# Kernel optimization log

Measured on AMD Instinct MI355X. Metric: run time of the kernel, lower is better.

Reference implementation:

```python
import jax, jax.numpy as jnp
import numpy as np

N_HEADS, D_MODEL, D_HEAD = 12, 768, 64
INIT_RANGE = 0.02
IGNORE = -100000.0

def setup_inputs() -> dict:
    key = jax.random.key(0)
    ks = jax.random.split(key, 5)
    x = jax.random.normal(ks[0], (4, 2048, D_MODEL), dtype=jnp.float32)
    W_Q = jax.random.normal(ks[1], (N_HEADS, D_MODEL, D_HEAD), dtype=jnp.float32) * INIT_RANGE
    W_K = jax.random.normal(ks[2], (N_HEADS, D_MODEL, D_HEAD), dtype=jnp.float32) * INIT_RANGE
    W_V = jax.random.normal(ks[3], (N_HEADS, D_MODEL, D_HEAD), dtype=jnp.float32) * INIT_RANGE
    W_O = jax.random.normal(ks[4], (N_HEADS, D_HEAD, D_MODEL), dtype=jnp.float32) * INIT_RANGE
    b_Q = jnp.zeros((N_HEADS, D_HEAD), dtype=jnp.float32)
    b_K = jnp.zeros((N_HEADS, D_HEAD), dtype=jnp.float32)
    b_V = jnp.zeros((N_HEADS, D_HEAD), dtype=jnp.float32)
    b_O = jnp.zeros((D_MODEL,), dtype=jnp.float32)
    return {"normalized_resid_pre": x, "W_Q": W_Q, "b_Q": b_Q, "W_K": W_K,
            "b_K": b_K, "W_V": W_V, "b_V": b_V, "W_O": W_O, "b_O": b_O}

def reference(normalized_resid_pre, W_Q, b_Q, W_K, b_K, W_V, b_V, W_O, b_O):
    x = normalized_resid_pre  # [b, s, d_model]
    q = jnp.einsum('bsd,hde->bshe', x, W_Q) + b_Q  # [b, s, h, d_head]
    k = jnp.einsum('bsd,hde->bshe', x, W_K) + b_K
    v = jnp.einsum('bsd,hde->bshe', x, W_V) + b_V
    scores = jnp.einsum('bqhe,bkhe->bhqk', q, k) / jnp.sqrt(jnp.float32(D_HEAD))
    S = x.shape[1]
    causal = jnp.triu(jnp.ones((S, S), dtype=bool), k=1)  # True above diagonal
    scores = jnp.where(causal, jnp.float32(IGNORE), scores)
    pattern = jax.nn.softmax(scores, axis=-1)  # [b, h, q, k]
    z = jnp.einsum('bhqk,bkhe->bqhe', pattern, v)
    attn_out = jnp.einsum('bqhe,hed->bqd', z, W_O) + b_O
    return attn_out
```

## Files before the change

kernel.cpp:

```cpp
#include <hip/hip_runtime.h>

typedef unsigned short u16;
typedef __bf16 bf16x8 __attribute__((ext_vector_type(8)));
typedef float f32x4 __attribute__((ext_vector_type(4)));

#define D_MODEL 768
#define NH 12
#define SEQ 2048
#define BB 4
#define QSCALE 0.18033688011112042f
#define FIXM 8.0f

__device__ __forceinline__ u16 f2b(float f) {
  __bf16 h = (__bf16)f;
  return __builtin_bit_cast(u16, h);
}

__device__ __forceinline__ void gload16(const void* g, void* l) {
  __builtin_amdgcn_global_load_lds((__attribute__((address_space(1))) void*)g,
                                   (__attribute__((address_space(3))) void*)l, 16, 0, 0);
}

__device__ __forceinline__ f32x4 mm16(bf16x8 a, bf16x8 b, f32x4 c) {
  return __builtin_amdgcn_mfma_f32_16x16x32_bf16(a, b, c, 0, 0, 0);
}

__global__ void prep_kernel(const float* __restrict__ x, const float* __restrict__ wq,
                            const float* __restrict__ wk, const float* __restrict__ wv,
                            const float* __restrict__ wo, const float* __restrict__ bq,
                            const float* __restrict__ bk, const float* __restrict__ bv,
                            u16* __restrict__ xb, u16* __restrict__ wt,
                            u16* __restrict__ wot, float* __restrict__ qkvb) {
  const int bid = blockIdx.x;
  if (bid < 6144) {
    int i = (bid * 256 + threadIdx.x) * 4;
    float4 v = *(const float4*)&x[i];
    ushort4 o;
    o.x = f2b(v.x); o.y = f2b(v.y); o.z = f2b(v.z); o.w = f2b(v.w);
    *(ushort4*)&xb[i] = o;
  } else {
    int i = (bid - 6144) * 256 + threadIdx.x;
    {
      int cp = i / 768, d = i % 768;
      int proj = cp / 768, c = cp % 768, h = c / 64, e = c % 64;
      const float* W = (proj == 0) ? wq : ((proj == 1) ? wk : wv);
      float v = W[(size_t)h * 49152 + d * 64 + e];
      if (proj == 0) v *= QSCALE;
      wt[i] = f2b(v);
    }
    if (i < 768 * 768) {
      int rp = i / 768, d = i % 768;
      wot[i] = f2b(wo[(size_t)d * 768 + rp]);
    }
    if (i < 2304) {
      int proj = i / 768, c = i % 768;
      float v = (proj == 0) ? bq[c] * QSCALE : ((proj == 1) ? bk[c] : bv[c]);
      qkvb[i] = v;
    }
  }
}

__global__ __launch_bounds__(512) void gemm_qkv_kernel(
    const u16* __restrict__ A, const u16* __restrict__ Bt,
    const float* __restrict__ qkvb, u16* __restrict__ qw, u16* __restrict__ kw,
    u16* __restrict__ vw) {
  __shared__ u16 lds[73728];
  const int tid = threadIdx.x;
  const int w = tid >> 6, lane = tid & 63;
  const int lg = lane >> 4, cl = lane & 15;
  const int L = blockIdx.x;
  const int v = (L & 7) * 72 + (L >> 3);
  const int bm = v % 9, bn = v / 9;
  const int wr = w >> 1, wc = w & 1;
  const int NT = 12;

  f32x4 vzero = {0.f, 0.f, 0.f, 0.f};
  f32x4 acc[4][4];
#pragma unroll
  for (int mi = 0; mi < 4; mi++)
#pragma unroll
    for (int ni = 0; ni < 4; ni++) acc[mi][ni] = vzero;

  const u16* aB = A + (size_t)bm * 256 * D_MODEL;
  const u16* bB = Bt + (size_t)bn * 128 * D_MODEL;
  const int l8 = lane >> 3, l7 = lane & 7;
  const int c7 = cl & 7;
  const int sw7 = l7 ^ l8;

  auto stage = [&](int buf, int kt, int half) {
    const int kof = kt * 64;
#pragma unroll
    for (int j2 = 0; j2 < 2; j2++) {
      const int r0 = (w * 4 + half * 2 + j2) * 8;
      gload16(aB + (size_t)(r0 + l8) * D_MODEL + kof + sw7 * 8,
              &lds[buf * 16384 + r0 * 64]);
    }
    const int r0b = (w * 2 + half) * 8;
    gload16(bB + (size_t)(r0b + l8) * D_MODEL + kof + sw7 * 8,
            &lds[49152 + buf * 8192 + r0b * 64]);
  };

  stage(0, 0, 0); stage(0, 0, 1);
  stage(1, 1, 0); stage(1, 1, 1);
  asm volatile("s_waitcnt vmcnt(6)" ::: "memory");
  __builtin_amdgcn_s_barrier();

  for (int kt = 0; kt < NT; ++kt) {
    const int cA = (kt % 3) * 16384;
    const int cB = 49152 + (kt % 3) * 8192;
    const int nbuf = (kt + 2) % 3;
#pragma unroll
    for (int ks = 0; ks < 2; ks++) {
      const int kc = (ks * 4 + lg) ^ c7;
      bf16x8 af[4], bf4[4];
#pragma unroll
      for (int mi = 0; mi < 4; mi++)
        af[mi] = *(const bf16x8*)&lds[cA + (wr * 64 + mi * 16 + cl) * 64 + kc * 8];
#pragma unroll
      for (int ni = 0; ni < 4; ni++)
        bf4[ni] = *(const bf16x8*)&lds[cB + (wc * 64 + ni * 16 + cl) * 64 + kc * 8];
      if (kt + 2 < NT) stage(nbuf, kt + 2, ks);
      if (ks == 1) {
        if (kt + 2 < NT) asm volatile("s_waitcnt vmcnt(6)" ::: "memory");
        else asm volatile("s_waitcnt vmcnt(0)" ::: "memory");
      }
      __builtin_amdgcn_s_barrier();
      __builtin_amdgcn_s_setprio(1);
#pragma unroll
      for (int mi = 0; mi < 4; mi++)
#pragma unroll
        for (int ni = 0; ni < 4; ni++)
          acc[mi][ni] = mm16(af[mi], bf4[ni], acc[mi][ni]);
      __builtin_amdgcn_s_setprio(0);
      __builtin_amdgcn_s_barrier();
    }
  }

  __syncthreads();
  u16* lw = &lds[w * 4096];
  const int cm = bm * 256 + wr * 64;
  const int cn = bn * 128 + wc * 64;
  const int proj = cm / 768;
  const int h = (cm % 768) >> 6;
  const int b = cn >> 11, s_base = cn & 2047;
  const int rlo = lane >> 3, q8 = lane & 7;

  float bz[4][4];
#pragma unroll
  for (int mi = 0; mi < 4; mi++) {
    float4 b4 = *(const float4*)&qkvb[cm + mi * 16 + lg * 4];
    bz[mi][0] = b4.x; bz[mi][1] = b4.y; bz[mi][2] = b4.z; bz[mi][3] = b4.w;
  }

  if (proj < 2) {
#pragma unroll
    for (int mi = 0; mi < 4; mi++) {
      const int e0 = mi * 16 + lg * 4;
#pragma unroll
      for (int ni = 0; ni < 4; ni++) {
        const int s_l = ni * 16 + cl;
        ushort4 pk;
        pk.x = f2b(acc[mi][ni][0] + bz[mi][0]);
        pk.y = f2b(acc[mi][ni][1] + bz[mi][1]);
        pk.z = f2b(acc[mi][ni][2] + bz[mi][2]);
        pk.w = f2b(acc[mi][ni][3] + bz[mi][3]);
        *(ushort4*)&lw[(s_l * 128 + ((e0 * 2) ^ ((s_l & 7) << 4))) >> 1] = pk;
      }
    }
    u16* dst = ((proj == 0) ? qw : kw) + (((size_t)(b * NH + h) * SEQ + s_base) << 6);
#pragma unroll
    for (int it = 0; it < 8; it++) {
      const int row = it * 8 + rlo;
      *(bf16x8*)&dst[row * 64 + q8 * 8] =
          *(const bf16x8*)&lw[(row * 128 + ((q8 * 16) ^ ((row & 7) << 4))) >> 1];
    }
  } else {
#pragma unroll
    for (int mi = 0; mi < 4; mi++)
#pragma unroll
      for (int ni = 0; ni < 4; ni++) {
        const int s_l = ni * 16 + cl;
#pragma unroll
        for (int r = 0; r < 4; r++) {
          const int e_l = mi * 16 + lg * 4 + r;
          lw[(e_l * 128 + ((s_l * 2) ^ ((e_l & 7) << 4))) >> 1] =
              f2b(acc[mi][ni][r] + bz[mi][r]);
        }
      }
    u16* dst = vw + (((size_t)(b * NH + h)) << 17) + s_base;
#pragma unroll
    for (int it = 0; it < 8; it++) {
      const int row = it * 8 + rlo;
      *(bf16x8*)&dst[((size_t)row << 11) + q8 * 8] =
          *(const bf16x8*)&lw[(row * 128 + ((q8 * 16) ^ ((row & 7) << 4))) >> 1];
    }
  }
}

__global__ __launch_bounds__(512) void gemm_out_kernel(
    const u16* __restrict__ A, const u16* __restrict__ Bt,
    const float* __restrict__ bias0, float* __restrict__ outf) {
  __shared__ u16 lds[73728];
  const int tid = threadIdx.x;
  const int w = tid >> 6, lane = tid & 63;
  const int lg = lane >> 4, cl = lane & 15;
  const int L = blockIdx.x;
  const int v = (L & 7) * 24 + (L >> 3);
  const int bm = v / 6, bn = v % 6;
  const int wr = w >> 1, wc = w & 1;
  const int NT = 12;

  f32x4 vzero = {0.f, 0.f, 0.f, 0.f};
  f32x4 acc[4][4];
#pragma unroll
  for (int mi = 0; mi < 4; mi++)
#pragma unroll
    for (int ni = 0; ni < 4; ni++) acc[mi][ni] = vzero;

  const u16* aB = A + (size_t)bm * 256 * D_MODEL;
  const u16* bB = Bt + (size_t)bn * 128 * D_MODEL;
  const int l8 = lane >> 3, l7 = lane & 7;
  const int c7 = cl & 7;
  const int sw7 = l7 ^ l8;

  auto stage = [&](int buf, int kt, int half) {
    const int kof = kt * 64;
#pragma unroll
    for (int j2 = 0; j2 < 2; j2++) {
      const int r0 = (w * 4 + half * 2 + j2) * 8;
      gload16(aB + (size_t)(r0 + l8) * D_MODEL + kof + sw7 * 8,
              &lds[buf * 16384 + r0 * 64]);
    }
    const int r0b = (w * 2 + half) * 8;
    gload16(bB + (size_t)(r0b + l8) * D_MODEL + kof + sw7 * 8,
            &lds[49152 + buf * 8192 + r0b * 64]);
  };

  stage(0, 0, 0); stage(0, 0, 1);
  stage(1, 1, 0); stage(1, 1, 1);
  asm volatile("s_waitcnt vmcnt(6)" ::: "memory");
  __builtin_amdgcn_s_barrier();

  for (int kt = 0; kt < NT; ++kt) {
    const int cA = (kt % 3) * 16384;
    const int cB = 49152 + (kt % 3) * 8192;
    const int nbuf = (kt + 2) % 3;
#pragma unroll
    for (int ks = 0; ks < 2; ks++) {
      const int kc = (ks * 4 + lg) ^ c7;
      bf16x8 af[4], bf4[4];
#pragma unroll
      for (int mi = 0; mi < 4; mi++)
        af[mi] = *(const bf16x8*)&lds[cA + (wr * 64 + mi * 16 + cl) * 64 + kc * 8];
#pragma unroll
      for (int ni = 0; ni < 4; ni++)
        bf4[ni] = *(const bf16x8*)&lds[cB + (wc * 64 + ni * 16 + cl) * 64 + kc * 8];
      if (kt + 2 < NT) stage(nbuf, kt + 2, ks);
      if (ks == 1) {
        if (kt + 2 < NT) asm volatile("s_waitcnt vmcnt(6)" ::: "memory");
        else asm volatile("s_waitcnt vmcnt(0)" ::: "memory");
      }
      __builtin_amdgcn_s_barrier();
      __builtin_amdgcn_s_setprio(1);
#pragma unroll
      for (int mi = 0; mi < 4; mi++)
#pragma unroll
        for (int ni = 0; ni < 4; ni++)
          acc[mi][ni] = mm16(af[mi], bf4[ni], acc[mi][ni]);
      __builtin_amdgcn_s_setprio(0);
      __builtin_amdgcn_s_barrier();
    }
  }

  __syncthreads();
  u16* lw = &lds[w * 4096];
  float* lwf = (float*)lw;
  const int m_base = bm * 256 + wr * 64;
  const int n0 = bn * 128 + wc * 64;
  const int rlo = lane >> 3, q8 = lane & 7;
#pragma unroll
  for (int hh = 0; hh < 2; hh++) {
#pragma unroll
    for (int nn = 0; nn < 2; nn++) {
      const int ni = hh * 2 + nn;
      const float bz = bias0[n0 + ni * 16 + cl];
      const int col = nn * 16 + cl;
#pragma unroll
      for (int mi = 0; mi < 4; mi++)
#pragma unroll
        for (int r = 0; r < 4; r++) {
          const int row = mi * 16 + lg * 4 + r;
          lwf[(row * 128 + ((col * 4) ^ ((row & 7) << 4))) >> 2] = acc[mi][ni][r] + bz;
        }
    }
#pragma unroll
    for (int it = 0; it < 8; it++) {
      const int row = it * 8 + rlo;
      const int byt = row * 128 + ((q8 * 16) ^ ((row & 7) << 4));
      *(float4*)&outf[(size_t)(m_base + row) * D_MODEL + n0 + hh * 32 + q8 * 4] =
          *(const float4*)((const char*)lwf + byt);
    }
  }
}

__global__ __launch_bounds__(512) void attn_kernel(
    const u16* __restrict__ q_ws, const u16* __restrict__ k_ws,
    const u16* __restrict__ vT_ws, u16* __restrict__ z_ws) {
  __shared__ u16 lk[2][4096];
  __shared__ u16 lv[2][4096];
  __shared__ u16 lp[8192];
  const int tid = threadIdx.x, w = tid >> 6, lane = tid & 63;
  const int lg = lane >> 4, cl = lane & 15, c7 = cl & 7;
  const int L = blockIdx.x;
  const int xcd = L & 7, i = L >> 3;
  const int p = 15 - (i / 6);
  const int bh = xcd * 6 + (i % 6);
  const u16* qp = q_ws + (size_t)bh * SEQ * 64;
  const u16* kp = k_ws + (size_t)bh * SEQ * 64;
  const u16* vp = vT_ws + (size_t)bh * 64 * SEQ;
  const int b = bh / NH, h = bh % NH;

  const __bf16 one1 = (__bf16)1.0f;
  const bf16x8 vones = {one1, one1, one1, one1, one1, one1, one1, one1};

  const int qbase = p * 128 + w * 16;
  const int qabs = qbase + cl;
  const int qtmax = 2 * p + 1;

  bf16x8 qf[2];
#pragma unroll
  for (int ks = 0; ks < 2; ks++)
    qf[ks] = *(const bf16x8*)&qp[(size_t)(qbase + cl) * 64 + ks * 32 + lg * 8];

  f32x4 vzero = {0.f, 0.f, 0.f, 0.f};
  f32x4 accO[4];
#pragma unroll
  for (int nb = 0; nb < 4; nb++) accO[nb] = vzero;
  f32x4 accS = vzero;

  gload16(kp + (size_t)(lane)*64 + w * 8, &lk[0][w * 64 * 8]);
  gload16(vp + (size_t)lane * SEQ + w * 8, &lv[0][w * 64 * 8]);
  asm volatile("s_waitcnt vmcnt(0)" ::: "memory");
  __builtin_amdgcn_s_barrier();

  for (int kt = 0; kt <= qtmax; ++kt) {
    const int cur = kt & 1;
    const int k0 = kt * 64;
    if (kt < qtmax) {
      const int kn = k0 + 64;
      gload16(kp + (size_t)(kn + lane) * 64 + w * 8, &lk[cur ^ 1][w * 64 * 8]);
      gload16(vp + (size_t)lane * SEQ + kn + w * 8, &lv[cur ^ 1][w * 64 * 8]);
    }

    f32x4 sa[4];
#pragma unroll
    for (int cb = 0; cb < 4; cb++) sa[cb] = vzero;
    __builtin_amdgcn_s_setprio(1);
#pragma unroll
    for (int ks = 0; ks < 2; ks++) {
#pragma unroll
      for (int cb = 0; cb < 4; cb++) {
        bf16x8 kf = *(const bf16x8*)&lk[cur][((ks * 4 + lg) * 64 + cb * 16 + cl) * 8];
        sa[cb] = mm16(kf, qf[ks], sa[cb]);
      }
    }
    __builtin_amdgcn_s_setprio(0);
    if (k0 + 63 > qabs) {
#pragma unroll
      for (int cb = 0; cb < 4; cb++)
#pragma unroll
        for (int r = 0; r < 4; r++)
          if (k0 + cb * 16 + lg * 4 + r > qabs) sa[cb][r] = -1e30f;
    }

#pragma unroll
    for (int cb = 0; cb < 4; cb++) {
      float p0 = __builtin_amdgcn_exp2f(sa[cb][0] - FIXM);
      float p1 = __builtin_amdgcn_exp2f(sa[cb][1] - FIXM);
      float p2 = __builtin_amdgcn_exp2f(sa[cb][2] - FIXM);
      float p3 = __builtin_amdgcn_exp2f(sa[cb][3] - FIXM);
      ushort4 pk;
      pk.x = f2b(p0); pk.y = f2b(p1); pk.z = f2b(p2); pk.w = f2b(p3);
      *(ushort4*)&lp[w * 1024 + (cl * 128 + ((cb * 32 + lg * 8) ^ (c7 << 4))) / 2] = pk;
    }

    __builtin_amdgcn_s_setprio(1);
#pragma unroll
    for (int ks = 0; ks < 2; ks++) {
      bf16x8 pf = *(const bf16x8*)&lp[w * 1024 +
                                      (cl * 128 + ((ks * 64 + lg * 16) ^ (c7 << 4))) / 2];
#pragma unroll
      for (int nb = 0; nb < 4; nb++) {
        bf16x8 vf = *(const bf16x8*)&lv[cur][((ks * 4 + lg) * 64 + nb * 16 + cl) * 8];
        accO[nb] = mm16(pf, vf, accO[nb]);
      }
      accS = mm16(pf, vones, accS);
    }
    __builtin_amdgcn_s_setprio(0);

    asm volatile("s_waitcnt vmcnt(0)" ::: "memory");
    __builtin_amdgcn_s_barrier();
  }

  float inv[4];
#pragma unroll
  for (int r = 0; r < 4; r++) inv[r] = 1.f / accS[r];
#pragma unroll
  for (int nb = 0; nb < 4; nb++)
#pragma unroll
    for (int r = 0; r < 4; r++) {
      const int qrow = qbase + lg * 4 + r;
      z_ws[((size_t)b * SEQ + qrow) * D_MODEL + h * 64 + nb * 16 + cl] =
          f2b(accO[nb][r] * inv[r]);
    }
}

extern "C" void kernel_launch(void* const* d_in, const int* in_sizes, int n_in,
                              void* d_out, int out_size, void* d_ws, size_t ws_size,
                              hipStream_t stream) {
  const float* x = (const float*)d_in[0];
  const float* wq = (const float*)d_in[1];
  const float* bq = (const float*)d_in[2];
  const float* wk = (const float*)d_in[3];
  const float* bk = (const float*)d_in[4];
  const float* wv = (const float*)d_in[5];
  const float* bv = (const float*)d_in[6];
  const float* wo = (const float*)d_in[7];
  const float* bo = (const float*)d_in[8];
  float* out = (float*)d_out;

  char* ws = (char*)d_ws;
  size_t off = 0;
  auto carve = [&](size_t bytes) -> u16* {
    u16* p = (u16*)(ws + off);
    off += (bytes + 255) & ~(size_t)255;
    return p;
  };
  u16* xb = carve((size_t)8192 * 768 * 2);
  u16* wt = carve((size_t)2304 * 768 * 2);
  u16* wot = carve((size_t)768 * 768 * 2);
  float* qkvb = (float*)carve((size_t)2304 * 4);
  u16* qw = carve((size_t)BB * NH * SEQ * 64 * 2);
  u16* kw = carve((size_t)BB * NH * SEQ * 64 * 2);
  u16* vw = carve((size_t)BB * NH * SEQ * 64 * 2);
  u16* zw = carve((size_t)8192 * 768 * 2);
  if (ws_size < off) return;

  prep_kernel<<<dim3(13056), dim3(256), 0, stream>>>(x, wq, wk, wv, wo, bq, bk, bv,
                                                     xb, wt, wot, qkvb);
  gemm_qkv_kernel<<<dim3(576), dim3(512), 0, stream>>>(wt, xb, qkvb, qw, kw, vw);
  attn_kernel<<<dim3(768), dim3(512), 0, stream>>>(qw, kw, vw, zw);
  gemm_out_kernel<<<dim3(192), dim3(512), 0, stream>>>(zw, wot, bo, out);
}
```

Measured before the change: 127.9 us.

## Halve attention block to 4 waves, each handling two 16-row query groups

The attention kernel now launches 256 threads instead of 512. Each wave processes two 16-row query groups (rows w*16 and w*16+64), so every K/V fragment read from LDS feeds two MFMAs. Staging of K/V tiles is split across 4 waves with two loads each. This cuts LDS K/V read traffic per MFMA and barrier participants, at the cost of doubled accumulator registers per wave and fewer waves available to hide latency.

```diff
diff --git a/kernel.cpp b/kernel.cpp
--- a/kernel.cpp
+++ b/kernel.cpp
@@ -303,7 +303,7 @@
   }
 }
 
-__global__ __launch_bounds__(512) void attn_kernel(
+__global__ __launch_bounds__(256) void attn_kernel(
     const u16* __restrict__ q_ws, const u16* __restrict__ k_ws,
     const u16* __restrict__ vT_ws, u16* __restrict__ z_ws) {
   __shared__ u16 lk[2][4096];
@@ -323,78 +323,98 @@
   const __bf16 one1 = (__bf16)1.0f;
   const bf16x8 vones = {one1, one1, one1, one1, one1, one1, one1, one1};
 
-  const int qbase = p * 128 + w * 16;
-  const int qabs = qbase + cl;
+  const int qb0 = p * 128 + w * 16;
   const int qtmax = 2 * p + 1;
 
-  bf16x8 qf[2];
-#pragma unroll
-  for (int ks = 0; ks < 2; ks++)
-    qf[ks] = *(const bf16x8*)&qp[(size_t)(qbase + cl) * 64 + ks * 32 + lg * 8];
+  bf16x8 qf[2][2];
+#pragma unroll
+  for (int g = 0; g < 2; g++)
+#pragma unroll
+    for (int ks = 0; ks < 2; ks++)
+      qf[g][ks] =
+          *(const bf16x8*)&qp[(size_t)(qb0 + g * 64 + cl) * 64 + ks * 32 + lg * 8];
 
   f32x4 vzero = {0.f, 0.f, 0.f, 0.f};
-  f32x4 accO[4];
-#pragma unroll
-  for (int nb = 0; nb < 4; nb++) accO[nb] = vzero;
-  f32x4 accS = vzero;
-
-  gload16(kp + (size_t)(lane)*64 + w * 8, &lk[0][w * 64 * 8]);
-  gload16(vp + (size_t)lane * SEQ + w * 8, &lv[0][w * 64 * 8]);
+  f32x4 accO[2][4];
+#pragma unroll
+  for (int g = 0; g < 2; g++)
+#pragma unroll
+    for (int nb = 0; nb < 4; nb++) accO[g][nb] = vzero;
+  f32x4 accS[2] = {vzero, vzero};
+
+  auto stage = [&](int buf, int kt) {
+    const int k0 = kt * 64;
+#pragma unroll
+    for (int c2 = 0; c2 < 2; c2++) {
+      const int ch = w + c2 * 4;
+      gload16(kp + (size_t)(k0 + lane) * 64 + ch * 8, &lk[buf][ch * 512]);
+      gload16(vp + (size_t)lane * SEQ + k0 + ch * 8, &lv[buf][ch * 512]);
+    }
+  };
+
+  stage(0, 0);
   asm volatile("s_waitcnt vmcnt(0)" ::: "memory");
   __builtin_amdgcn_s_barrier();
 
   for (int kt = 0; kt <= qtmax; ++kt) {
     const int cur = kt & 1;
     const int k0 = kt * 64;
-    if (kt < qtmax) {
-      const int kn = k0 + 64;
-      gload16(kp + (size_t)(kn + lane) * 64 + w * 8, &lk[cur ^ 1][w * 64 * 8]);
-      gload16(vp + (size_t)lane * SEQ + kn + w * 8, &lv[cur ^ 1][w * 64 * 8]);
-    }
-
-    f32x4 sa[4];
-#pragma unroll
-    for (int cb = 0; cb < 4; cb++) sa[cb] = vzero;
+    if (kt < qtmax) stage(cur ^ 1, kt + 1);
+
+    f32x4 sa[2][4];
+#pragma unroll
+    for (int g = 0; g < 2; g++)
+#pragma unroll
+      for (int cb = 0; cb < 4; cb++) sa[g][cb] = vzero;
     __builtin_amdgcn_s_setprio(1);
 #pragma unroll
     for (int ks = 0; ks < 2; ks++) {
 #pragma unroll
       for (int cb = 0; cb < 4; cb++) {
         bf16x8 kf = *(const bf16x8*)&lk[cur][((ks * 4 + lg) * 64 + cb * 16 + cl) * 8];
-        sa[cb] = mm16(kf, qf[ks], sa[cb]);
+        sa[0][cb] = mm16(kf, qf[0][ks], sa[0][cb]);
+        sa[1][cb] = mm16(kf, qf[1][ks], sa[1][cb]);
       }
     }
     __builtin_amdgcn_s_setprio(0);
-    if (k0 + 63 > qabs) {
-#pragma unroll
-      for (int cb = 0; cb < 4; cb++)
-#pragma unroll
-        for (int r = 0; r < 4; r++)
-          if (k0 + cb * 16 + lg * 4 + r > qabs) sa[cb][r] = -1e30f;
-    }
-
-#pragma unroll
-    for (int cb = 0; cb < 4; cb++) {
-      float p0 = __builtin_amdgcn_exp2f(sa[cb][0] - FIXM);
-      float p1 = __builtin_amdgcn_exp2f(sa[cb][1] - FIXM);
-      float p2 = __builtin_amdgcn_exp2f(sa[cb][2] - FIXM);
-      float p3 = __builtin_amdgcn_exp2f(sa[cb][3] - FIXM);
-      ushort4 pk;
-      pk.x = f2b(p0); pk.y = f2b(p1); pk.z = f2b(p2); pk.w = f2b(p3);
-      *(ushort4*)&lp[w * 1024 + (cl * 128 + ((cb * 32 + lg * 8) ^ (c7 << 4))) / 2] = pk;
+
+#pragma unroll
+    for (int g = 0; g < 2; g++) {
+      const int qa = qb0 + g * 64 + cl;
+      if (k0 + 63 > qa) {
+#pragma unroll
+        for (int cb = 0; cb < 4; cb++)
+#pragma unroll
+          for (int r = 0; r < 4; r++)
+            if (k0 + cb * 16 + lg * 4 + r > qa) sa[g][cb][r] = -1e30f;
+      }
+#pragma unroll
+      for (int cb = 0; cb < 4; cb++) {
+        float p0 = __builtin_amdgcn_exp2f(sa[g][cb][0] - FIXM);
+        float p1 = __builtin_amdgcn_exp2f(sa[g][cb][1] - FIXM);
+        float p2 = __builtin_amdgcn_exp2f(sa[g][cb][2] - FIXM);
+        float p3 = __builtin_amdgcn_exp2f(sa[g][cb][3] - FIXM);
+        ushort4 pk;
+        pk.x = f2b(p0); pk.y = f2b(p1); pk.z = f2b(p2); pk.w = f2b(p3);
+        *(ushort4*)&lp[(w * 2 + g) * 1024 +
+                       (cl * 128 + ((cb * 32 + lg * 8) ^ (c7 << 4))) / 2] = pk;
+      }
     }
 
     __builtin_amdgcn_s_setprio(1);
 #pragma unroll
     for (int ks = 0; ks < 2; ks++) {
-      bf16x8 pf = *(const bf16x8*)&lp[w * 1024 +
-                                      (cl * 128 + ((ks * 64 + lg * 16) ^ (c7 << 4))) / 2];
+      const int pof = (cl * 128 + ((ks * 64 + lg * 16) ^ (c7 << 4))) / 2;
+      bf16x8 pf0 = *(const bf16x8*)&lp[(w * 2 + 0) * 1024 + pof];
+      bf16x8 pf1 = *(const bf16x8*)&lp[(w * 2 + 1) * 1024 + pof];
 #pragma unroll
       for (int nb = 0; nb < 4; nb++) {
         bf16x8 vf = *(const bf16x8*)&lv[cur][((ks * 4 + lg) * 64 + nb * 16 + cl) * 8];
-        accO[nb] = mm16(pf, vf, accO[nb]);
-      }
-      accS = mm16(pf, vones, accS);
+        accO[0][nb] = mm16(pf0, vf, accO[0][nb]);
+        accO[1][nb] = mm16(pf1, vf, accO[1][nb]);
+      }
+      accS[0] = mm16(pf0, vones, accS[0]);
+      accS[1] = mm16(pf1, vones, accS[1]);
     }
     __builtin_amdgcn_s_setprio(0);
 
@@ -402,17 +422,20 @@
     __builtin_amdgcn_s_barrier();
   }
 
-  float inv[4];
-#pragma unroll
-  for (int r = 0; r < 4; r++) inv[r] = 1.f / accS[r];
-#pragma unroll
-  for (int nb = 0; nb < 4; nb++)
-#pragma unroll
-    for (int r = 0; r < 4; r++) {
-      const int qrow = qbase + lg * 4 + r;
-      z_ws[((size_t)b * SEQ + qrow) * D_MODEL + h * 64 + nb * 16 + cl] =
-          f2b(accO[nb][r] * inv[r]);
-    }
+#pragma unroll
+  for (int g = 0; g < 2; g++) {
+    float inv[4];
+#pragma unroll
+    for (int r = 0; r < 4; r++) inv[r] = 1.f / accS[g][r];
+#pragma unroll
+    for (int nb = 0; nb < 4; nb++)
+#pragma unroll
+      for (int r = 0; r < 4; r++) {
+        const int qrow = qb0 + g * 64 + lg * 4 + r;
+        z_ws[((size_t)b * SEQ + qrow) * D_MODEL + h * 64 + nb * 16 + cl] =
+            f2b(accO[g][nb][r] * inv[r]);
+      }
+  }
 }
 
 extern "C" void kernel_launch(void* const* d_in, const int* in_sizes, int n_in,
@@ -449,6 +472,6 @@
   prep_kernel<<<dim3(13056), dim3(256), 0, stream>>>(x, wq, wk, wv, wo, bq, bk, bv,
                                                      xb, wt, wot, qkvb);
   gemm_qkv_kernel<<<dim3(576), dim3(512), 0, stream>>>(wt, xb, qkvb, qw, kw, vw);
-  attn_kernel<<<dim3(768), dim3(512), 0, stream>>>(qw, kw, vw, zw);
+  attn_kernel<<<dim3(768), dim3(256), 0, stream>>>(qw, kw, vw, zw);
   gemm_out_kernel<<<dim3(192), dim3(512), 0, stream>>>(zw, wot, bo, out);
 }
```

After: 138.4 us. +8.3%, slower.
